# Optimization experiments

Hardware: AMD Instinct MI355X
Metric: run time of the kernel (lower is better)

## Reference

```python
import jax, jax.numpy as jnp
import numpy as np
from jax import lax

N = 2048
T = 512
B = 32
IN_SIZE = 1
OUT_SIZE = 1

DT = 1e-4
U_CONST = 0.3
TAU = 0.008
TAU_F = 1.5
TAU_D = 0.3
ALPHA = 1.5
I_B = 8.0
J_EI = 1.1
J_IE = 2.2


def setup_inputs() -> dict:
    key = jax.random.key(0)
    k1, k2, k3, k4 = jax.random.split(key, 4)
    inp = jax.random.normal(k1, (T, B, IN_SIZE), dtype=jnp.float32)
    W_in = jax.random.normal(k2, (N, IN_SIZE), dtype=jnp.float32) / jnp.sqrt(jnp.float32(IN_SIZE))
    # J is nn.Parameter(zeros) pre-training; use small random init so dynamics are non-trivial
    J = jax.random.normal(k3, (N, N), dtype=jnp.float32) / jnp.sqrt(jnp.float32(N))
    W_out = jax.random.normal(k4, (OUT_SIZE, N), dtype=jnp.float32) / jnp.sqrt(jnp.float32(N))
    return {"inp": inp, "W_in": W_in, "J": J, "W_out": W_out}


def _rate(h):
    # R(h) = alpha * ln(1 + exp(h/alpha))  == Softplus(beta=1/alpha)
    return ALPHA * jax.nn.softplus(h / ALPHA)


def reference(inp, W_in, J, W_out):
    seq_len, batch, _ = inp.shape
    n = J.shape[0]

    def step(state, inp_t):
        h, u, x, h_I = state                      # [B,N],[B,N],[B,N],[B,1]
        I_e = inp_t @ W_in.T                      # [B,N] (N_in == N, pad width 0)
        R = _rate(h)
        R_I = _rate(h_I)
        syn = (u * x * R) @ J.T                   # matmul(J, (uxR)^T)^T
        dh = (-h + syn + I_B + I_e) / TAU - J_EI * R_I / TAU  # N_in == N: applies to all units
        du = (U_CONST - u) / TAU_F + U_CONST * (1.0 - u) * R
        dx = (1.0 - x) / TAU_D - u * x * R
        dh_I = (-h_I + J_IE * jnp.sum(R, axis=1, keepdims=True)) / TAU
        h2 = h + dh * DT
        u2 = u + du * DT
        x2 = x + dx * DT
        h_I2 = h_I + dh_I * DT
        out = _rate(h2) @ W_out.T                 # out_slice = h2[:, -N_out:] == full h2
        return (h2, u2, x2, h_I2), (h2, u2, x2, h_I2, out)

    h0 = jnp.zeros((batch, n), dtype=inp.dtype)
    u0 = jnp.full((batch, n), U_CONST, dtype=inp.dtype)
    x0 = jnp.ones((batch, n), dtype=inp.dtype)
    hI0 = jnp.zeros((batch, 1), dtype=inp.dtype)

    _, (all_h, all_u, all_x, all_hI, outputs) = lax.scan(step, (h0, u0, x0, hI0), inp)
    return (all_h, all_u, all_x, all_hI, outputs)
```

## Files before the change

kernel.cpp:

```cpp
#include <hip/hip_runtime.h>

#define N_ 2048
#define T_ 512
#define B_ 32
#define NWG 64
#define NS 32
#define DT_ 1e-4f
#define U_CONST_ 0.3f
#define TAU_F_ 1.5f
#define TAU_D_ 0.3f
#define ALPHA_ 1.5f
#define I_B_ 8.0f
#define J_EI_ 1.1f
#define J_IE_ 2.2f
#define INV_TAU 125.0f
#define INV_ALPHA (1.0f/1.5f)
#define LO_SCALE 4096.0f
#define INV_LO_SCALE 2.44140625e-4f

#define U_OFF  (512ull*32*2048)
#define X_OFF  (2ull*512*32*2048)
#define HI_OFF (3ull*512*32*2048)
#define OUT_OFF (HI_OFF + 512ull*32)

typedef _Float16 half8 __attribute__((ext_vector_type(8)));
typedef float f32x4 __attribute__((ext_vector_type(4)));
typedef unsigned long long u64;
typedef u64 u64x2 __attribute__((ext_vector_type(2)));

__device__ u64   g_vh[2][(B_*N_)/4];
__device__ u64   g_vl[2][(B_*N_)/4];
__device__ float g_rp[2][B_*NWG];
__device__ unsigned g_flags[NWG*16];

#define SYS_LD_U64(p)   __hip_atomic_load((p), __ATOMIC_RELAXED, __HIP_MEMORY_SCOPE_SYSTEM)
#define SYS_LD_F32(p)   __hip_atomic_load((p), __ATOMIC_RELAXED, __HIP_MEMORY_SCOPE_SYSTEM)
#define SYS_LD_U32(p)   __hip_atomic_load((p), __ATOMIC_RELAXED, __HIP_MEMORY_SCOPE_SYSTEM)
#define SYS_ST_U32(p,v) __hip_atomic_store((p), (v), __ATOMIC_RELAXED, __HIP_MEMORY_SCOPE_SYSTEM)
#define SYS_ST_F32(p,v) __hip_atomic_store((p), (v), __ATOMIC_RELAXED, __HIP_MEMORY_SCOPE_SYSTEM)

__device__ inline float rate_f(float h) {
  float z = h * INV_ALPHA;
  return ALPHA_ * (fmaxf(z, 0.0f) + log1pf(expf(-fabsf(z))));
}

__device__ inline unsigned packpair(float a, float b, float scale_into_lo, bool lo_plane) {
  return 0;
}

__global__ void init_kernel() {
  g_flags[threadIdx.x] = 0u;
}

__global__ __launch_bounds__(256, 1) void stp_kernel(
    const float* __restrict__ inp, const float* __restrict__ W_in,
    const float* __restrict__ J, float* __restrict__ out)
{
  const int tid  = threadIdx.x;
  const int wg   = blockIdx.x;
  const int wave = tid >> 6;
  const int lane = tid & 63;

  __shared__ float sh_C[4][1024];
  __shared__ float sh_part[256];
  __shared__ float sh_hI[32], sh_RI[32], sh_inp[32];

  half8 jh[2][16], jl[2][16];
  {
    const int r = lane & 15, q = lane >> 4;
    #pragma unroll
    for (int nt = 0; nt < 2; ++nt)
      #pragma unroll
      for (int c = 0; c < 16; ++c) {
        const float* src = J + (size_t)(wg*NS + nt*16 + r) * N_ + wave*512 + c*32 + q*8;
        half8 hv, lv;
        #pragma unroll
        for (int j = 0; j < 8; ++j) {
          float f = src[j];
          _Float16 hi = (_Float16)f;
          _Float16 lo = (_Float16)((f - (float)hi) * LO_SCALE);
          hv[j] = hi; lv[j] = lo;
        }
        jh[nt][c] = hv; jl[nt][c] = lv;
      }
  }

  const int np = tid & 15;
  const int n0 = wg*NS + 2*np;
  const int bq = tid >> 4;
  const float w0 = W_in[n0], w1 = W_in[n0+1];

  float hh[2][2], uu[2][2], xx[2][2];
  #pragma unroll
  for (int c = 0; c < 2; ++c)
    #pragma unroll
    for (int j = 0; j < 2; ++j) { hh[c][j] = 0.0f; uu[c][j] = U_CONST_; xx[c][j] = 1.0f; }

  if (tid < 32) sh_hI[tid] = 0.0f;
  __syncthreads();

  for (int t = 0; t < T_; ++t) {
    const int pb = t & 1;
    unsigned* vhd = (unsigned*)g_vh[pb];
    unsigned* vld = (unsigned*)g_vl[pb];

    #pragma unroll
    for (int c = 0; c < 2; ++c) {
      const int b = bq + 16*c;
      float R0 = rate_f(hh[c][0]), R1 = rate_f(hh[c][1]);
      float v0 = uu[c][0]*xx[c][0]*R0, v1 = uu[c][1]*xx[c][1]*R1;
      _Float16 h0 = (_Float16)v0, h1 = (_Float16)v1;
      _Float16 l0 = (_Float16)((v0 - (float)h0) * LO_SCALE);
      _Float16 l1 = (_Float16)((v1 - (float)h1) * LO_SCALE);
      unsigned hp = (unsigned)__builtin_bit_cast(unsigned short, h0)
                  | ((unsigned)__builtin_bit_cast(unsigned short, h1) << 16);
      unsigned lp = (unsigned)__builtin_bit_cast(unsigned short, l0)
                  | ((unsigned)__builtin_bit_cast(unsigned short, l1) << 16);
      const unsigned idx = (unsigned)(b*N_ + n0) >> 1;
      SYS_ST_U32(vhd + idx, hp);
      SYS_ST_U32(vld + idx, lp);
      uu[c][0] += ((U_CONST_-uu[c][0])*(1.0f/TAU_F_) + U_CONST_*(1.0f-uu[c][0])*R0)*DT_;
      uu[c][1] += ((U_CONST_-uu[c][1])*(1.0f/TAU_F_) + U_CONST_*(1.0f-uu[c][1])*R1)*DT_;
      xx[c][0] += ((1.0f-xx[c][0])*(1.0f/TAU_D_) - v0)*DT_;
      xx[c][1] += ((1.0f-xx[c][1])*(1.0f/TAU_D_) - v1)*DT_;
      float s = R0 + R1;
      s += __shfl_xor(s, 1); s += __shfl_xor(s, 2);
      s += __shfl_xor(s, 4); s += __shfl_xor(s, 8);
      if ((lane & 15) == 0) SYS_ST_F32(&g_rp[pb][b*NWG + wg], s);
    }

    __syncthreads();
    if (tid == 0) SYS_ST_U32(&g_flags[wg*16], (unsigned)(t + 1));

    #pragma unroll
    for (int c = 0; c < 2; ++c) {
      const int b = bq + 16*c;
      const size_t o = (size_t)t*(B_*N_) + (size_t)b*N_ + n0;
      *(float2*)&out[U_OFF + o] = make_float2(uu[c][0], uu[c][1]);
      *(float2*)&out[X_OFF + o] = make_float2(xx[c][0], xx[c][1]);
    }
    if (tid < 32) sh_inp[tid] = inp[t*B_ + tid];

    if (wave == 0) {
      const unsigned target = (unsigned)(t + 1);
      while (true) {
        unsigned f = SYS_LD_U32(&g_flags[lane*16]);
        if (__ballot(f >= target) == ~0ull) break;
        __builtin_amdgcn_s_sleep(1);
      }
    }
    __syncthreads();
    __atomic_signal_fence(__ATOMIC_ACQUIRE);

    {
      const int b2 = tid & 31, gc = tid >> 5;
      float s = 0.0f;
      #pragma unroll
      for (int k = 0; k < 8; ++k)
        s += SYS_LD_F32(&g_rp[pb][b2*NWG + gc*8 + k]);
      sh_part[gc*32 + b2] = s;
    }

    {
      const int r = lane & 15, q = lane >> 4;
      f32x4 aH00 = {0,0,0,0}, aH01 = {0,0,0,0}, aH10 = {0,0,0,0}, aH11 = {0,0,0,0};
      f32x4 aL00 = {0,0,0,0}, aL01 = {0,0,0,0}, aL10 = {0,0,0,0}, aL11 = {0,0,0,0};
      const int base0 = (r*N_      + wave*512 + q*8) >> 2;
      const int base1 = ((r+16)*N_ + wave*512 + q*8) >> 2;
      #pragma unroll
      for (int c = 0; c < 16; ++c) {
        const int o0 = base0 + c*8, o1 = base1 + c*8;
        u64x2 th0 = { SYS_LD_U64(&g_vh[pb][o0]), SYS_LD_U64(&g_vh[pb][o0+1]) };
        u64x2 tl0 = { SYS_LD_U64(&g_vl[pb][o0]), SYS_LD_U64(&g_vl[pb][o0+1]) };
        u64x2 th1 = { SYS_LD_U64(&g_vh[pb][o1]), SYS_LD_U64(&g_vh[pb][o1+1]) };
        u64x2 tl1 = { SYS_LD_U64(&g_vl[pb][o1]), SYS_LD_U64(&g_vl[pb][o1+1]) };
        half8 ah0 = __builtin_bit_cast(half8, th0);
        half8 al0 = __builtin_bit_cast(half8, tl0);
        half8 ah1 = __builtin_bit_cast(half8, th1);
        half8 al1 = __builtin_bit_cast(half8, tl1);
        aH00 = __builtin_amdgcn_mfma_f32_16x16x32_f16(ah0, jh[0][c], aH00, 0, 0, 0);
        aH01 = __builtin_amdgcn_mfma_f32_16x16x32_f16(ah0, jh[1][c], aH01, 0, 0, 0);
        aH10 = __builtin_amdgcn_mfma_f32_16x16x32_f16(ah1, jh[0][c], aH10, 0, 0, 0);
        aH11 = __builtin_amdgcn_mfma_f32_16x16x32_f16(ah1, jh[1][c], aH11, 0, 0, 0);
        aL00 = __builtin_amdgcn_mfma_f32_16x16x32_f16(ah0, jl[0][c], aL00, 0, 0, 0);
        aL00 = __builtin_amdgcn_mfma_f32_16x16x32_f16(al0, jh[0][c], aL00, 0, 0, 0);
        aL01 = __builtin_amdgcn_mfma_f32_16x16x32_f16(ah0, jl[1][c], aL01, 0, 0, 0);
        aL01 = __builtin_amdgcn_mfma_f32_16x16x32_f16(al0, jh[1][c], aL01, 0, 0, 0);
        aL10 = __builtin_amdgcn_mfma_f32_16x16x32_f16(ah1, jl[0][c], aL10, 0, 0, 0);
        aL10 = __builtin_amdgcn_mfma_f32_16x16x32_f16(al1, jh[0][c], aL10, 0, 0, 0);
        aL11 = __builtin_amdgcn_mfma_f32_16x16x32_f16(ah1, jl[1][c], aL11, 0, 0, 0);
        aL11 = __builtin_amdgcn_mfma_f32_16x16x32_f16(al1, jh[1][c], aL11, 0, 0, 0);
      }
      #pragma unroll
      for (int i = 0; i < 4; ++i) {
        int row = q*4 + i;
        sh_C[wave][ row     *32      + r] = aH00[i] + INV_LO_SCALE*aL00[i];
        sh_C[wave][ row     *32 + 16 + r] = aH01[i] + INV_LO_SCALE*aL01[i];
        sh_C[wave][(row+16) *32      + r] = aH10[i] + INV_LO_SCALE*aL10[i];
        sh_C[wave][(row+16) *32 + 16 + r] = aH11[i] + INV_LO_SCALE*aL11[i];
      }
    }
    __syncthreads();

    if (tid < 32) {
      float s = 0.0f;
      #pragma unroll
      for (int gc = 0; gc < 8; ++gc) s += sh_part[gc*32 + tid];
      float hI = sh_hI[tid];
      sh_RI[tid] = rate_f(hI);
      float hI2 = hI + DT_*INV_TAU*(-hI + J_IE_*s);
      sh_hI[tid] = hI2;
      if (wg == 0) out[HI_OFF + (size_t)t*B_ + tid] = hI2;
    }
    __syncthreads();

    #pragma unroll
    for (int c = 0; c < 2; ++c) {
      const int b = bq + 16*c;
      const int e = b*32 + 2*np;
      float sy0 = sh_C[0][e]   + sh_C[1][e]   + sh_C[2][e]   + sh_C[3][e];
      float sy1 = sh_C[0][e+1] + sh_C[1][e+1] + sh_C[2][e+1] + sh_C[3][e+1];
      float ib = sh_inp[b];
      float ri = J_EI_*INV_TAU*sh_RI[b];
      float dh0 = (-hh[c][0] + sy0 + I_B_ + ib*w0)*INV_TAU - ri;
      float dh1 = (-hh[c][1] + sy1 + I_B_ + ib*w1)*INV_TAU - ri;
      hh[c][0] += dh0*DT_;
      hh[c][1] += dh1*DT_;
      *(float2*)&out[(size_t)t*(B_*N_) + (size_t)b*N_ + n0] = make_float2(hh[c][0], hh[c][1]);
    }
  }
}

__global__ __launch_bounds__(256) void out_kernel(
    const float* __restrict__ allh, const float* __restrict__ W_out,
    float* __restrict__ outp)
{
  const int bid = blockIdx.x;
  const int tid = threadIdx.x;
  __shared__ float red[4];
  const float* hrow = allh + (size_t)bid * N_;
  float s = 0.0f;
  #pragma unroll
  for (int i = 0; i < 8; ++i) {
    int n = tid + 256*i;
    s += rate_f(hrow[n]) * W_out[n];
  }
  s += __shfl_xor(s, 32); s += __shfl_xor(s, 16); s += __shfl_xor(s, 8);
  s += __shfl_xor(s, 4);  s += __shfl_xor(s, 2);  s += __shfl_xor(s, 1);
  if ((tid & 63) == 0) red[tid >> 6] = s;
  __syncthreads();
  if (tid == 0) outp[bid] = red[0] + red[1] + red[2] + red[3];
}

extern "C" void kernel_launch(void* const* d_in, const int* in_sizes, int n_in,
                              void* d_out, int out_size, void* d_ws, size_t ws_size,
                              hipStream_t stream)
{
  const float* inp   = (const float*)d_in[0];
  const float* W_in  = (const float*)d_in[1];
  const float* J     = (const float*)d_in[2];
  const float* W_out = (const float*)d_in[3];
  float* out = (float*)d_out;

  hipLaunchKernelGGL(init_kernel, dim3(1), dim3(NWG*16), 0, stream);
  hipLaunchKernelGGL(stp_kernel, dim3(NWG), dim3(256), 0, stream,
                     inp, W_in, J, out);
  hipLaunchKernelGGL(out_kernel, dim3(T_*B_), dim3(256), 0, stream,
                     out, W_out, out + OUT_OFF);
}
```

Before: 10.27 ms.

## Replace persistent grid-barrier kernel with per-timestep kernel launches

Drops the persistent 64-workgroup kernel, which held J in registers and synchronised timesteps with global flag spinning. J is now pre-split into fp16 hi/lo planes in global memory by a prep kernel, and one step kernel with 128 workgroups is launched per timestep. State is reloaded from the output buffer each step, and kernel boundaries replace the spin barrier. This adds 512 launch overheads and rereads 16MB of fp16 J from L2/HBM every step instead of keeping it in registers.

```diff
diff --git a/kernel.cpp b/kernel.cpp
--- a/kernel.cpp
+++ b/kernel.cpp
@@ -3,8 +3,6 @@
 #define N_ 2048
 #define T_ 512
 #define B_ 32
-#define NWG 64
-#define NS 32
 #define DT_ 1e-4f
 #define U_CONST_ 0.3f
 #define TAU_F_ 1.5f
@@ -27,208 +25,162 @@
 typedef float f32x4 __attribute__((ext_vector_type(4)));
 typedef unsigned long long u64;
 typedef u64 u64x2 __attribute__((ext_vector_type(2)));
-
+typedef unsigned u32;
+
+__device__ _Float16 Jh[(size_t)N_*N_];
+__device__ _Float16 Jl[(size_t)N_*N_];
 __device__ u64   g_vh[2][(B_*N_)/4];
 __device__ u64   g_vl[2][(B_*N_)/4];
-__device__ float g_rp[2][B_*NWG];
-__device__ unsigned g_flags[NWG*16];
-
-#define SYS_LD_U64(p)   __hip_atomic_load((p), __ATOMIC_RELAXED, __HIP_MEMORY_SCOPE_SYSTEM)
-#define SYS_LD_F32(p)   __hip_atomic_load((p), __ATOMIC_RELAXED, __HIP_MEMORY_SCOPE_SYSTEM)
-#define SYS_LD_U32(p)   __hip_atomic_load((p), __ATOMIC_RELAXED, __HIP_MEMORY_SCOPE_SYSTEM)
-#define SYS_ST_U32(p,v) __hip_atomic_store((p), (v), __ATOMIC_RELAXED, __HIP_MEMORY_SCOPE_SYSTEM)
-#define SYS_ST_F32(p,v) __hip_atomic_store((p), (v), __ATOMIC_RELAXED, __HIP_MEMORY_SCOPE_SYSTEM)
+__device__ float g_rp[2][B_*64];
 
 __device__ inline float rate_f(float h) {
   float z = h * INV_ALPHA;
   return ALPHA_ * (fmaxf(z, 0.0f) + log1pf(expf(-fabsf(z))));
 }
 
-__device__ inline unsigned packpair(float a, float b, float scale_into_lo, bool lo_plane) {
-  return 0;
-}
-
-__global__ void init_kernel() {
-  g_flags[threadIdx.x] = 0u;
-}
-
-__global__ __launch_bounds__(256, 1) void stp_kernel(
+__global__ __launch_bounds__(256) void prep_kernel(const float* __restrict__ J)
+{
+  const int idx = blockIdx.x*256 + threadIdx.x;
+  for (size_t i = idx; i < (size_t)N_*N_; i += 65536) {
+    float f = J[i];
+    _Float16 hi = (_Float16)f;
+    Jh[i] = hi;
+    Jl[i] = (_Float16)((f - (float)hi) * LO_SCALE);
+  }
+  const float R0 = rate_f(0.0f);
+  const float v0 = U_CONST_ * 1.0f * R0;
+  _Float16 h0 = (_Float16)v0;
+  _Float16 l0 = (_Float16)((v0 - (float)h0) * LO_SCALE);
+  u32 hp = (u32)__builtin_bit_cast(unsigned short, h0); hp |= hp << 16;
+  u32 lp = (u32)__builtin_bit_cast(unsigned short, l0); lp |= lp << 16;
+  if (idx < (B_*N_)/2) {
+    ((u32*)g_vh[0])[idx] = hp;
+    ((u32*)g_vl[0])[idx] = lp;
+  }
+  if (idx < B_*64) g_rp[0][idx] = 32.0f * R0;
+}
+
+__global__ __launch_bounds__(256) void step_kernel(
     const float* __restrict__ inp, const float* __restrict__ W_in,
-    const float* __restrict__ J, float* __restrict__ out)
+    float* __restrict__ out, int t)
 {
   const int tid  = threadIdx.x;
-  const int wg   = blockIdx.x;
+  const int nt   = blockIdx.x & 63;
+  const int bt   = blockIdx.x >> 6;
   const int wave = tid >> 6;
   const int lane = tid & 63;
-
-  __shared__ float sh_C[4][1024];
-  __shared__ float sh_part[256];
-  __shared__ float sh_hI[32], sh_RI[32], sh_inp[32];
-
-  half8 jh[2][16], jl[2][16];
+  const int ns = nt*32, bs = bt*16;
+  const int sl = t & 1;
+
+  __shared__ float sh_C[4][512];
+
+  const int m  = tid >> 4;
+  const int np = tid & 15;
+  const int b  = bs + m;
+  const int n0 = ns + 2*np;
+
+  const bool first = (t == 0);
+  const size_t prev = (size_t)(t-1)*(B_*N_) + (size_t)b*N_ + n0;
+
+  float2 hv, uv, xv;
+  float hI;
+  if (first) {
+    hv = make_float2(0.0f, 0.0f);
+    uv = make_float2(U_CONST_, U_CONST_);
+    xv = make_float2(1.0f, 1.0f);
+    hI = 0.0f;
+  } else {
+    hv = *(const float2*)&out[prev];
+    uv = *(const float2*)&out[U_OFF + prev];
+    xv = *(const float2*)&out[X_OFF + prev];
+    hI = out[HI_OFF + (size_t)(t-1)*B_ + b];
+  }
+  const float ib = inp[t*B_ + b];
+  const float w0 = W_in[n0], w1 = W_in[n0+1];
+
   {
     const int r = lane & 15, q = lane >> 4;
+    const u64* vhp = g_vh[sl];
+    const u64* vlp = g_vl[sl];
+    const int abase = ((bs + r)*N_ + wave*512 + q*8) >> 2;
+    const _Float16* jh0p = &Jh[(size_t)(ns + r)*N_      + wave*512 + q*8];
+    const _Float16* jh1p = &Jh[(size_t)(ns + 16 + r)*N_ + wave*512 + q*8];
+    const _Float16* jl0p = &Jl[(size_t)(ns + r)*N_      + wave*512 + q*8];
+    const _Float16* jl1p = &Jl[(size_t)(ns + 16 + r)*N_ + wave*512 + q*8];
+    f32x4 aH0 = {0,0,0,0}, aH1 = {0,0,0,0};
+    f32x4 aL0 = {0,0,0,0}, aL1 = {0,0,0,0};
     #pragma unroll
-    for (int nt = 0; nt < 2; ++nt)
-      #pragma unroll
-      for (int c = 0; c < 16; ++c) {
-        const float* src = J + (size_t)(wg*NS + nt*16 + r) * N_ + wave*512 + c*32 + q*8;
-        half8 hv, lv;
-        #pragma unroll
-        for (int j = 0; j < 8; ++j) {
-          float f = src[j];
-          _Float16 hi = (_Float16)f;
-          _Float16 lo = (_Float16)((f - (float)hi) * LO_SCALE);
-          hv[j] = hi; lv[j] = lo;
-        }
-        jh[nt][c] = hv; jl[nt][c] = lv;
-      }
-  }
-
-  const int np = tid & 15;
-  const int n0 = wg*NS + 2*np;
-  const int bq = tid >> 4;
-  const float w0 = W_in[n0], w1 = W_in[n0+1];
-
-  float hh[2][2], uu[2][2], xx[2][2];
-  #pragma unroll
-  for (int c = 0; c < 2; ++c)
+    for (int c = 0; c < 16; ++c) {
+      const int o = abase + c*8;
+      u64x2 th = *(const u64x2*)(vhp + o);
+      u64x2 tl = *(const u64x2*)(vlp + o);
+      half8 ah = __builtin_bit_cast(half8, th);
+      half8 al = __builtin_bit_cast(half8, tl);
+      half8 j0 = *(const half8*)(jh0p + c*32);
+      half8 j1 = *(const half8*)(jh1p + c*32);
+      half8 k0 = *(const half8*)(jl0p + c*32);
+      half8 k1 = *(const half8*)(jl1p + c*32);
+      aH0 = __builtin_amdgcn_mfma_f32_16x16x32_f16(ah, j0, aH0, 0, 0, 0);
+      aH1 = __builtin_amdgcn_mfma_f32_16x16x32_f16(ah, j1, aH1, 0, 0, 0);
+      aL0 = __builtin_amdgcn_mfma_f32_16x16x32_f16(ah, k0, aL0, 0, 0, 0);
+      aL0 = __builtin_amdgcn_mfma_f32_16x16x32_f16(al, j0, aL0, 0, 0, 0);
+      aL1 = __builtin_amdgcn_mfma_f32_16x16x32_f16(ah, k1, aL1, 0, 0, 0);
+      aL1 = __builtin_amdgcn_mfma_f32_16x16x32_f16(al, j1, aL1, 0, 0, 0);
+    }
     #pragma unroll
-    for (int j = 0; j < 2; ++j) { hh[c][j] = 0.0f; uu[c][j] = U_CONST_; xx[c][j] = 1.0f; }
-
-  if (tid < 32) sh_hI[tid] = 0.0f;
+    for (int i = 0; i < 4; ++i) {
+      int row = q*4 + i;
+      sh_C[wave][row*32      + r] = aH0[i] + INV_LO_SCALE*aL0[i];
+      sh_C[wave][row*32 + 16 + r] = aH1[i] + INV_LO_SCALE*aL1[i];
+    }
+  }
+
+  if (nt == 0 && tid < 16) {
+    const int bb = bs + tid;
+    float S = 0.0f;
+    #pragma unroll
+    for (int k2 = 0; k2 < 64; ++k2) S += g_rp[sl][bb*64 + k2];
+    float hIt = first ? 0.0f : out[HI_OFF + (size_t)(t-1)*B_ + bb];
+    out[HI_OFF + (size_t)t*B_ + bb] = hIt + DT_*INV_TAU*(-hIt + J_IE_*S);
+  }
   __syncthreads();
 
-  for (int t = 0; t < T_; ++t) {
-    const int pb = t & 1;
-    unsigned* vhd = (unsigned*)g_vh[pb];
-    unsigned* vld = (unsigned*)g_vl[pb];
-
-    #pragma unroll
-    for (int c = 0; c < 2; ++c) {
-      const int b = bq + 16*c;
-      float R0 = rate_f(hh[c][0]), R1 = rate_f(hh[c][1]);
-      float v0 = uu[c][0]*xx[c][0]*R0, v1 = uu[c][1]*xx[c][1]*R1;
-      _Float16 h0 = (_Float16)v0, h1 = (_Float16)v1;
-      _Float16 l0 = (_Float16)((v0 - (float)h0) * LO_SCALE);
-      _Float16 l1 = (_Float16)((v1 - (float)h1) * LO_SCALE);
-      unsigned hp = (unsigned)__builtin_bit_cast(unsigned short, h0)
-                  | ((unsigned)__builtin_bit_cast(unsigned short, h1) << 16);
-      unsigned lp = (unsigned)__builtin_bit_cast(unsigned short, l0)
-                  | ((unsigned)__builtin_bit_cast(unsigned short, l1) << 16);
-      const unsigned idx = (unsigned)(b*N_ + n0) >> 1;
-      SYS_ST_U32(vhd + idx, hp);
-      SYS_ST_U32(vld + idx, lp);
-      uu[c][0] += ((U_CONST_-uu[c][0])*(1.0f/TAU_F_) + U_CONST_*(1.0f-uu[c][0])*R0)*DT_;
-      uu[c][1] += ((U_CONST_-uu[c][1])*(1.0f/TAU_F_) + U_CONST_*(1.0f-uu[c][1])*R1)*DT_;
-      xx[c][0] += ((1.0f-xx[c][0])*(1.0f/TAU_D_) - v0)*DT_;
-      xx[c][1] += ((1.0f-xx[c][1])*(1.0f/TAU_D_) - v1)*DT_;
-      float s = R0 + R1;
-      s += __shfl_xor(s, 1); s += __shfl_xor(s, 2);
-      s += __shfl_xor(s, 4); s += __shfl_xor(s, 8);
-      if ((lane & 15) == 0) SYS_ST_F32(&g_rp[pb][b*NWG + wg], s);
-    }
-
-    __syncthreads();
-    if (tid == 0) SYS_ST_U32(&g_flags[wg*16], (unsigned)(t + 1));
-
-    #pragma unroll
-    for (int c = 0; c < 2; ++c) {
-      const int b = bq + 16*c;
-      const size_t o = (size_t)t*(B_*N_) + (size_t)b*N_ + n0;
-      *(float2*)&out[U_OFF + o] = make_float2(uu[c][0], uu[c][1]);
-      *(float2*)&out[X_OFF + o] = make_float2(xx[c][0], xx[c][1]);
-    }
-    if (tid < 32) sh_inp[tid] = inp[t*B_ + tid];
-
-    if (wave == 0) {
-      const unsigned target = (unsigned)(t + 1);
-      while (true) {
-        unsigned f = SYS_LD_U32(&g_flags[lane*16]);
-        if (__ballot(f >= target) == ~0ull) break;
-        __builtin_amdgcn_s_sleep(1);
-      }
-    }
-    __syncthreads();
-    __atomic_signal_fence(__ATOMIC_ACQUIRE);
-
-    {
-      const int b2 = tid & 31, gc = tid >> 5;
-      float s = 0.0f;
-      #pragma unroll
-      for (int k = 0; k < 8; ++k)
-        s += SYS_LD_F32(&g_rp[pb][b2*NWG + gc*8 + k]);
-      sh_part[gc*32 + b2] = s;
-    }
-
-    {
-      const int r = lane & 15, q = lane >> 4;
-      f32x4 aH00 = {0,0,0,0}, aH01 = {0,0,0,0}, aH10 = {0,0,0,0}, aH11 = {0,0,0,0};
-      f32x4 aL00 = {0,0,0,0}, aL01 = {0,0,0,0}, aL10 = {0,0,0,0}, aL11 = {0,0,0,0};
-      const int base0 = (r*N_      + wave*512 + q*8) >> 2;
-      const int base1 = ((r+16)*N_ + wave*512 + q*8) >> 2;
-      #pragma unroll
-      for (int c = 0; c < 16; ++c) {
-        const int o0 = base0 + c*8, o1 = base1 + c*8;
-        u64x2 th0 = { SYS_LD_U64(&g_vh[pb][o0]), SYS_LD_U64(&g_vh[pb][o0+1]) };
-        u64x2 tl0 = { SYS_LD_U64(&g_vl[pb][o0]), SYS_LD_U64(&g_vl[pb][o0+1]) };
-        u64x2 th1 = { SYS_LD_U64(&g_vh[pb][o1]), SYS_LD_U64(&g_vh[pb][o1+1]) };
-        u64x2 tl1 = { SYS_LD_U64(&g_vl[pb][o1]), SYS_LD_U64(&g_vl[pb][o1+1]) };
-        half8 ah0 = __builtin_bit_cast(half8, th0);
-        half8 al0 = __builtin_bit_cast(half8, tl0);
-        half8 ah1 = __builtin_bit_cast(half8, th1);
-        half8 al1 = __builtin_bit_cast(half8, tl1);
-        aH00 = __builtin_amdgcn_mfma_f32_16x16x32_f16(ah0, jh[0][c], aH00, 0, 0, 0);
-        aH01 = __builtin_amdgcn_mfma_f32_16x16x32_f16(ah0, jh[1][c], aH01, 0, 0, 0);
-        aH10 = __builtin_amdgcn_mfma_f32_16x16x32_f16(ah1, jh[0][c], aH10, 0, 0, 0);
-        aH11 = __builtin_amdgcn_mfma_f32_16x16x32_f16(ah1, jh[1][c], aH11, 0, 0, 0);
-        aL00 = __builtin_amdgcn_mfma_f32_16x16x32_f16(ah0, jl[0][c], aL00, 0, 0, 0);
-        aL00 = __builtin_amdgcn_mfma_f32_16x16x32_f16(al0, jh[0][c], aL00, 0, 0, 0);
-        aL01 = __builtin_amdgcn_mfma_f32_16x16x32_f16(ah0, jl[1][c], aL01, 0, 0, 0);
-        aL01 = __builtin_amdgcn_mfma_f32_16x16x32_f16(al0, jh[1][c], aL01, 0, 0, 0);
-        aL10 = __builtin_amdgcn_mfma_f32_16x16x32_f16(ah1, jl[0][c], aL10, 0, 0, 0);
-        aL10 = __builtin_amdgcn_mfma_f32_16x16x32_f16(al1, jh[0][c], aL10, 0, 0, 0);
-        aL11 = __builtin_amdgcn_mfma_f32_16x16x32_f16(ah1, jl[1][c], aL11, 0, 0, 0);
-        aL11 = __builtin_amdgcn_mfma_f32_16x16x32_f16(al1, jh[1][c], aL11, 0, 0, 0);
-      }
-      #pragma unroll
-      for (int i = 0; i < 4; ++i) {
-        int row = q*4 + i;
-        sh_C[wave][ row     *32      + r] = aH00[i] + INV_LO_SCALE*aL00[i];
-        sh_C[wave][ row     *32 + 16 + r] = aH01[i] + INV_LO_SCALE*aL01[i];
-        sh_C[wave][(row+16) *32      + r] = aH10[i] + INV_LO_SCALE*aL10[i];
-        sh_C[wave][(row+16) *32 + 16 + r] = aH11[i] + INV_LO_SCALE*aL11[i];
-      }
-    }
-    __syncthreads();
-
-    if (tid < 32) {
-      float s = 0.0f;
-      #pragma unroll
-      for (int gc = 0; gc < 8; ++gc) s += sh_part[gc*32 + tid];
-      float hI = sh_hI[tid];
-      sh_RI[tid] = rate_f(hI);
-      float hI2 = hI + DT_*INV_TAU*(-hI + J_IE_*s);
-      sh_hI[tid] = hI2;
-      if (wg == 0) out[HI_OFF + (size_t)t*B_ + tid] = hI2;
-    }
-    __syncthreads();
-
-    #pragma unroll
-    for (int c = 0; c < 2; ++c) {
-      const int b = bq + 16*c;
-      const int e = b*32 + 2*np;
-      float sy0 = sh_C[0][e]   + sh_C[1][e]   + sh_C[2][e]   + sh_C[3][e];
-      float sy1 = sh_C[0][e+1] + sh_C[1][e+1] + sh_C[2][e+1] + sh_C[3][e+1];
-      float ib = sh_inp[b];
-      float ri = J_EI_*INV_TAU*sh_RI[b];
-      float dh0 = (-hh[c][0] + sy0 + I_B_ + ib*w0)*INV_TAU - ri;
-      float dh1 = (-hh[c][1] + sy1 + I_B_ + ib*w1)*INV_TAU - ri;
-      hh[c][0] += dh0*DT_;
-      hh[c][1] += dh1*DT_;
-      *(float2*)&out[(size_t)t*(B_*N_) + (size_t)b*N_ + n0] = make_float2(hh[c][0], hh[c][1]);
-    }
-  }
+  const int e = m*32 + 2*np;
+  float sy0 = sh_C[0][e]   + sh_C[1][e]   + sh_C[2][e]   + sh_C[3][e];
+  float sy1 = sh_C[0][e+1] + sh_C[1][e+1] + sh_C[2][e+1] + sh_C[3][e+1];
+
+  float R0 = rate_f(hv.x), R1 = rate_f(hv.y);
+  float v0 = uv.x*xv.x*R0, v1 = uv.y*xv.y*R1;
+  float u20 = uv.x + ((U_CONST_-uv.x)*(1.0f/TAU_F_) + U_CONST_*(1.0f-uv.x)*R0)*DT_;
+  float u21 = uv.y + ((U_CONST_-uv.y)*(1.0f/TAU_F_) + U_CONST_*(1.0f-uv.y)*R1)*DT_;
+  float x20 = xv.x + ((1.0f-xv.x)*(1.0f/TAU_D_) - v0)*DT_;
+  float x21 = xv.y + ((1.0f-xv.y)*(1.0f/TAU_D_) - v1)*DT_;
+  float ri  = J_EI_*INV_TAU*rate_f(hI);
+  float h20 = hv.x + ((-hv.x + sy0 + I_B_ + ib*w0)*INV_TAU - ri)*DT_;
+  float h21 = hv.y + ((-hv.y + sy1 + I_B_ + ib*w1)*INV_TAU - ri)*DT_;
+
+  const size_t cur = (size_t)t*(B_*N_) + (size_t)b*N_ + n0;
+  *(float2*)&out[cur]         = make_float2(h20, h21);
+  *(float2*)&out[U_OFF + cur] = make_float2(u20, u21);
+  *(float2*)&out[X_OFF + cur] = make_float2(x20, x21);
+
+  float R20 = rate_f(h20), R21 = rate_f(h21);
+  float nv0 = u20*x20*R20, nv1 = u21*x21*R21;
+  _Float16 p0 = (_Float16)nv0, p1 = (_Float16)nv1;
+  _Float16 q0 = (_Float16)((nv0 - (float)p0) * LO_SCALE);
+  _Float16 q1 = (_Float16)((nv1 - (float)p1) * LO_SCALE);
+  u32 hp = (u32)__builtin_bit_cast(unsigned short, p0)
+         | ((u32)__builtin_bit_cast(unsigned short, p1) << 16);
+  u32 lp = (u32)__builtin_bit_cast(unsigned short, q0)
+         | ((u32)__builtin_bit_cast(unsigned short, q1) << 16);
+  const unsigned vidx = (unsigned)(b*N_ + n0) >> 1;
+  ((u32*)g_vh[sl^1])[vidx] = hp;
+  ((u32*)g_vl[sl^1])[vidx] = lp;
+
+  float s = R20 + R21;
+  s += __shfl_xor(s, 1); s += __shfl_xor(s, 2);
+  s += __shfl_xor(s, 4); s += __shfl_xor(s, 8);
+  if (np == 0) g_rp[sl^1][b*64 + nt] = s;
 }
 
 __global__ __launch_bounds__(256) void out_kernel(
@@ -262,9 +214,10 @@
   const float* W_out = (const float*)d_in[3];
   float* out = (float*)d_out;
 
-  hipLaunchKernelGGL(init_kernel, dim3(1), dim3(NWG*16), 0, stream);
-  hipLaunchKernelGGL(stp_kernel, dim3(NWG), dim3(256), 0, stream,
-                     inp, W_in, J, out);
+  hipLaunchKernelGGL(prep_kernel, dim3(256), dim3(256), 0, stream, J);
+  for (int t = 0; t < T_; ++t)
+    hipLaunchKernelGGL(step_kernel, dim3(128), dim3(256), 0, stream,
+                       inp, W_in, out, t);
   hipLaunchKernelGGL(out_kernel, dim3(T_*B_), dim3(256), 0, stream,
                      out, W_out, out + OUT_OFF);
 }
```

After: 8.630 ms. -16.0%, faster.
